# Optimization experiments

Hardware: AMD Instinct MI355X
Metric: run time of the kernel (lower is better)

The kernel has to match this reference:

```python
import jax, jax.numpy as jnp
import numpy as np

NUM_BINS = 500
DOSE_MIN = 0.0
DOSE_MAX = 75.0
SHAPE = (4, 1, 128, 128, 128)


def setup_inputs() -> dict:
    key = jax.random.key(0)
    k1, k2, k3 = jax.random.split(key, 3)
    d_pred = jax.random.uniform(k1, SHAPE, jnp.float32) * DOSE_MAX
    d_gt = jax.random.uniform(k2, SHAPE, jnp.float32) * DOSE_MAX
    mask = (jax.random.uniform(k3, SHAPE, jnp.float32) < 0.3).astype(jnp.float32)
    return {"d_pred": d_pred, "d_gt": d_gt, "mask": mask}


def _compute_dvh(dose_masked, mask, bins):
    # dose_masked, mask: [B, N]; bins: [K] sorted thresholds.
    # frac_k = sum_n mask_n * 1[dose_n >= t_k] / (sum_n mask_n + 1e-6)
    # c_n = #bins t <= dose_n  (side='right' includes equality, matching >=),
    # so 1[dose_n >= t_k] == 1[c_n > k]. Build a mask-weighted histogram of c
    # over [0, K] and take the reverse-cumulative tail.
    K = bins.shape[0]
    c = jnp.searchsorted(bins, dose_masked, side="right")  # [B, N] ints in [0, K]
    hist = jax.vmap(
        lambda cc, mm: jnp.zeros(K + 1, mm.dtype).at[cc].add(mm)
    )(c, mask)  # [B, K+1]
    tail = jnp.cumsum(hist[:, ::-1], axis=1)[:, ::-1]  # tail[:, j] = sum_{i>=j} hist[:, i]
    count_ge = tail[:, 1:]  # [B, K]: count of (masked) voxels with dose >= t_k
    denom = jnp.sum(mask, axis=1, keepdims=True) + 1e-6
    return count_ge / denom


def reference(d_pred, d_gt, mask):
    bins = jnp.linspace(DOSE_MIN, DOSE_MAX, NUM_BINS)
    B = d_pred.shape[0]
    m = mask.reshape(B, -1)
    dp = d_pred.reshape(B, -1) * m
    dg = d_gt.reshape(B, -1) * m
    dvh_pred = _compute_dvh(dp, m, bins)  # [B, K]
    dvh_gt = _compute_dvh(dg, m, bins)    # [B, K]
    return jnp.mean((dvh_pred - dvh_gt) ** 2)
```

## Files before the change

kernel.cpp:

```cpp
#include <hip/hip_runtime.h>
#include <stdint.h>


#define NBINS 500
#define NHIST 501
#define BATCH 4
#define NPB (1 << 21)
#define VPB (NPB / 4)
#define THREADS 512
#define WAVES 8
#define BLOCKS_PER_BATCH 256
#define STRIDE (BLOCKS_PER_BATCH * THREADS)

#define MC_OFF 2048
#define WS_INTS 2052

__device__ __forceinline__ int bin_of(float d) {
    const float STEP = 75.0f / 499.0f;
    const float INV  = 499.0f / 75.0f;
    int k = (int)(d * INV);
    if (k > 499) k = 499;
    if ((float)k * STEP > d) --k;
    else if (k < 499 && (float)(k + 1) * STEP <= d) ++k;
    if ((float)k * STEP > d) --k;
    return k + 1;
}

__global__ __launch_bounds__(THREADS) void dvh_hist_kernel(
        const float4* __restrict__ dp, const float4* __restrict__ dg,
        const float4* __restrict__ dm, int* __restrict__ ws) {
    __shared__ int shd[WAVES * 512];
    __shared__ unsigned int smc;
    const int b = blockIdx.y;
    const int t = threadIdx.x;
    const int wbase = (t >> 6) << 9;

    #pragma unroll
    for (int i = 0; i < WAVES; ++i) shd[i * THREADS + t] = 0;
    if (t == 0) smc = 0u;
    __syncthreads();

    const size_t base = (size_t)b * VPB + blockIdx.x * THREADS + t;
    float4 m0 = dm[base];              float4 m1 = dm[base + STRIDE];
    float4 m2 = dm[base + 2 * STRIDE]; float4 m3 = dm[base + 3 * STRIDE];
    float4 p0 = dp[base];              float4 p1 = dp[base + STRIDE];
    float4 p2 = dp[base + 2 * STRIDE]; float4 p3 = dp[base + 3 * STRIDE];
    float4 g0 = dg[base];              float4 g1 = dg[base + STRIDE];
    float4 g2 = dg[base + 2 * STRIDE]; float4 g3 = dg[base + 3 * STRIDE];

    unsigned int myc = 0;
#define DO(mm, pp, gg) \
    if (mm != 0.0f) { atomicAdd(&shd[wbase + bin_of(pp)], 1); \
                      atomicAdd(&shd[wbase + bin_of(gg)], -1); ++myc; }
    DO(m0.x, p0.x, g0.x) DO(m0.y, p0.y, g0.y) DO(m0.z, p0.z, g0.z) DO(m0.w, p0.w, g0.w)
    DO(m1.x, p1.x, g1.x) DO(m1.y, p1.y, g1.y) DO(m1.z, p1.z, g1.z) DO(m1.w, p1.w, g1.w)
    DO(m2.x, p2.x, g2.x) DO(m2.y, p2.y, g2.y) DO(m2.z, p2.z, g2.z) DO(m2.w, p2.w, g2.w)
    DO(m3.x, p3.x, g3.x) DO(m3.y, p3.y, g3.y) DO(m3.z, p3.z, g3.z) DO(m3.w, p3.w, g3.w)
#undef DO
    if (myc) atomicAdd(&smc, myc);
    __syncthreads();

    if (t < NHIST) {
        int v = 0;
        #pragma unroll
        for (int w = 0; w < WAVES; ++w) v += shd[w * 512 + t];
        if (v) atomicAdd(&ws[b * 512 + t], v);
    }
    if (t == 0 && smc) atomicAdd((unsigned int*)&ws[MC_OFF + b], smc);
}

__global__ __launch_bounds__(512) void dvh_reduce_kernel(
        const int* __restrict__ ws, float* __restrict__ out) {
    __shared__ int wtot[8];
    __shared__ float facc[8];
    const int t = threadIdx.x;
    const int lane = t & 63;
    const int w = t >> 6;
    float acc = 0.0f;

    for (int b = 0; b < BATCH; ++b) {
        int v = (t < NHIST) ? ws[b * 512 + t] : 0;
        #pragma unroll
        for (int off = 1; off < 64; off <<= 1) {
            int n = __shfl_up(v, off, 64);
            if (lane >= off) v += n;
        }
        if (lane == 63) wtot[w] = v;
        __syncthreads();
        int offset = 0, total = 0;
        #pragma unroll
        for (int i = 0; i < 8; ++i) {
            int x = wtot[i];
            total += x;
            if (i < w) offset += x;
        }
        const int prefix = v + offset;
        const float denom = (float)((unsigned int)ws[MC_OFF + b]) + 1e-6f;
        if (t < NBINS) {
            float diff = (float)(total - prefix) / denom;
            acc += diff * diff;
        }
        __syncthreads();
    }

    #pragma unroll
    for (int off = 32; off > 0; off >>= 1) acc += __shfl_down(acc, off, 64);
    if (lane == 0) facc[w] = acc;
    __syncthreads();
    if (t == 0) {
        float s = 0.0f;
        #pragma unroll
        for (int i = 0; i < 8; ++i) s += facc[i];
        out[0] = s * (1.0f / (BATCH * NBINS));
    }
}

extern "C" void kernel_launch(void* const* d_in, const int* in_sizes, int n_in,
                              void* d_out, int out_size, void* d_ws, size_t ws_size,
                              hipStream_t stream) {
    const float4* dp = (const float4*)d_in[0];
    const float4* dg = (const float4*)d_in[1];
    const float4* dm = (const float4*)d_in[2];
    int* ws = (int*)d_ws;

    hipMemsetAsync(d_ws, 0, WS_INTS * sizeof(int), stream);

    dim3 grid(BLOCKS_PER_BATCH, BATCH);
    dvh_hist_kernel<<<grid, dim3(THREADS), 0, stream>>>(dp, dg, dm, ws);
    dvh_reduce_kernel<<<1, dim3(512), 0, stream>>>(ws, (float*)d_out);
}
```

Baseline: 128.1 us.

## Fuse histogram and reduction kernels via last-block-done counter

Merges the histogram kernel and the single-block reduction kernel into one launch. An atomic completion counter and a threadfence let the last finishing block run the prefix-sum and squared-error reduction. The per-block shared-memory atomic on the mask count becomes a wave shuffle reduction followed by one global atomic per wave. This removes one kernel launch and its gap, in exchange for a fence and an extra global atomic in every block.

```diff
diff --git a/kernel.cpp b/kernel.cpp
--- a/kernel.cpp
+++ b/kernel.cpp
@@ -10,10 +10,12 @@
 #define THREADS 512
 #define WAVES 8
 #define BLOCKS_PER_BATCH 256
+#define TOTAL_BLOCKS (BLOCKS_PER_BATCH * BATCH)
 #define STRIDE (BLOCKS_PER_BATCH * THREADS)
 
 #define MC_OFF 2048
-#define WS_INTS 2052
+#define DONE_OFF 2052
+#define WS_INTS 2053
 
 __device__ __forceinline__ int bin_of(float d) {
     const float STEP = 75.0f / 499.0f;
@@ -26,21 +28,29 @@
     return k + 1;
 }
 
-__global__ __launch_bounds__(THREADS) void dvh_hist_kernel(
+__device__ __forceinline__ int ws_load(const int* p) {
+    return __hip_atomic_load(p, __ATOMIC_RELAXED, __HIP_MEMORY_SCOPE_AGENT);
+}
+
+__global__ __launch_bounds__(THREADS) void dvh_fused_kernel(
         const float4* __restrict__ dp, const float4* __restrict__ dg,
-        const float4* __restrict__ dm, int* __restrict__ ws) {
+        const float4* __restrict__ dm, int* __restrict__ ws,
+        float* __restrict__ out) {
     __shared__ int shd[WAVES * 512];
-    __shared__ unsigned int smc;
+    __shared__ int slast;
+    __shared__ int wtot[WAVES];
+    __shared__ float facc[WAVES];
     const int b = blockIdx.y;
     const int t = threadIdx.x;
-    const int wbase = (t >> 6) << 9;
+    const int lane = t & 63;
+    const int w = t >> 6;
+    const int wbase = w << 9;
 
     #pragma unroll
-    for (int i = 0; i < WAVES; ++i) shd[i * THREADS + t] = 0;
-    if (t == 0) smc = 0u;
+    for (int i = 0; i < WAVES; ++i) shd[i * 512 + t] = 0;
     __syncthreads();
 
-    const size_t base = (size_t)b * VPB + blockIdx.x * THREADS + t;
+    const size_t base = (size_t)b * VPB + (size_t)blockIdx.x * THREADS + t;
     float4 m0 = dm[base];              float4 m1 = dm[base + STRIDE];
     float4 m2 = dm[base + 2 * STRIDE]; float4 m3 = dm[base + 3 * STRIDE];
     float4 p0 = dp[base];              float4 p1 = dp[base + STRIDE];
@@ -57,29 +67,30 @@
     DO(m2.x, p2.x, g2.x) DO(m2.y, p2.y, g2.y) DO(m2.z, p2.z, g2.z) DO(m2.w, p2.w, g2.w)
     DO(m3.x, p3.x, g3.x) DO(m3.y, p3.y, g3.y) DO(m3.z, p3.z, g3.z) DO(m3.w, p3.w, g3.w)
 #undef DO
-    if (myc) atomicAdd(&smc, myc);
+    #pragma unroll
+    for (int off = 32; off > 0; off >>= 1) myc += __shfl_down(myc, off, 64);
     __syncthreads();
 
     if (t < NHIST) {
         int v = 0;
         #pragma unroll
-        for (int w = 0; w < WAVES; ++w) v += shd[w * 512 + t];
+        for (int i = 0; i < WAVES; ++i) v += shd[i * 512 + t];
         if (v) atomicAdd(&ws[b * 512 + t], v);
     }
-    if (t == 0 && smc) atomicAdd((unsigned int*)&ws[MC_OFF + b], smc);
-}
+    if (lane == 0 && myc) atomicAdd(&ws[MC_OFF + b], (int)myc);
 
-__global__ __launch_bounds__(512) void dvh_reduce_kernel(
-        const int* __restrict__ ws, float* __restrict__ out) {
-    __shared__ int wtot[8];
-    __shared__ float facc[8];
-    const int t = threadIdx.x;
-    const int lane = t & 63;
-    const int w = t >> 6;
+    __threadfence();
+    __syncthreads();
+    if (t == 0) {
+        int old = atomicAdd(&ws[DONE_OFF], 1);
+        slast = (old == TOTAL_BLOCKS - 1) ? 1 : 0;
+    }
+    __syncthreads();
+    if (!slast) return;
+
     float acc = 0.0f;
-
-    for (int b = 0; b < BATCH; ++b) {
-        int v = (t < NHIST) ? ws[b * 512 + t] : 0;
+    for (int bb = 0; bb < BATCH; ++bb) {
+        int v = (t < NHIST) ? ws_load(&ws[bb * 512 + t]) : 0;
         #pragma unroll
         for (int off = 1; off < 64; off <<= 1) {
             int n = __shfl_up(v, off, 64);
@@ -89,13 +100,13 @@
         __syncthreads();
         int offset = 0, total = 0;
         #pragma unroll
-        for (int i = 0; i < 8; ++i) {
+        for (int i = 0; i < WAVES; ++i) {
             int x = wtot[i];
             total += x;
             if (i < w) offset += x;
         }
         const int prefix = v + offset;
-        const float denom = (float)((unsigned int)ws[MC_OFF + b]) + 1e-6f;
+        const float denom = (float)ws_load(&ws[MC_OFF + bb]) + 1e-6f;
         if (t < NBINS) {
             float diff = (float)(total - prefix) / denom;
             acc += diff * diff;
@@ -110,7 +121,7 @@
     if (t == 0) {
         float s = 0.0f;
         #pragma unroll
-        for (int i = 0; i < 8; ++i) s += facc[i];
+        for (int i = 0; i < WAVES; ++i) s += facc[i];
         out[0] = s * (1.0f / (BATCH * NBINS));
     }
 }
@@ -126,6 +137,5 @@
     hipMemsetAsync(d_ws, 0, WS_INTS * sizeof(int), stream);
 
     dim3 grid(BLOCKS_PER_BATCH, BATCH);
-    dvh_hist_kernel<<<grid, dim3(THREADS), 0, stream>>>(dp, dg, dm, ws);
-    dvh_reduce_kernel<<<1, dim3(512), 0, stream>>>(ws, (float*)d_out);
+    dvh_fused_kernel<<<grid, dim3(THREADS), 0, stream>>>(dp, dg, dm, ws, (float*)d_out);
 }
```

After: 356.4 us. 2.78x slower.
